# Kernel tuning notes

Hardware: AMD Instinct MI355X
Metric: run time of the kernel (lower is better)

The kernel has to match this reference:

```python
import jax, jax.numpy as jnp
import numpy as np

B, L, D = 4, 2048, 1024


def setup_inputs() -> dict:
    key = jax.random.key(0)
    ks = jax.random.split(key, 7)
    scale = 1.0 / np.sqrt(D)
    x = jax.random.normal(ks[0], (B, L, D), dtype=jnp.float32)
    wq = jax.random.normal(ks[1], (D, D), dtype=jnp.float32) * scale
    wk = jax.random.normal(ks[2], (D, D), dtype=jnp.float32) * scale
    wv = jax.random.normal(ks[3], (D, D), dtype=jnp.float32) * scale
    bq = jnp.zeros((D,), dtype=jnp.float32)
    bk = jnp.zeros((D,), dtype=jnp.float32)
    bv = jnp.zeros((D,), dtype=jnp.float32)
    # causal decoder mask, shape [B, 1, L, L] as produced by nn.make_causal_mask
    causal = jnp.tril(jnp.ones((L, L), dtype=bool))
    mask = jnp.broadcast_to(causal[None, None, :, :], (B, 1, L, L))
    return {"x": x, "mask": mask, "wq": wq, "bq": bq, "wk": wk, "bk": bk, "wv": wv, "bv": bv}


def reference(x, mask, wq, bq, wk, bk, wv, bv):
    # q/k/v projections (Dense with bias)
    q = x @ wq + bq            # [B, L, D]
    k = x @ wk + bk
    v = x @ wv + bv
    depth = q.shape[-1]
    q = q / jnp.sqrt(jnp.asarray(depth, dtype=q.dtype))
    attn = jnp.einsum('bqd,bkd->bqk', q, k)          # [B, L, L]
    attn = jnp.where(jnp.squeeze(mask), attn, -999999)
    attn = jax.nn.softmax(attn, axis=-1)
    out = attn @ v                                    # [B, L, D]
    return out
```

## Files before the change

### kernel.cpp

```cpp
#include <hip/hip_runtime.h>

typedef __bf16 bf16_t;
typedef __attribute__((ext_vector_type(8))) __bf16 bf16x8;
typedef __attribute__((ext_vector_type(4))) __bf16 bf16x4;
typedef __attribute__((ext_vector_type(4))) float f32x4;

#define B_  4
#define L_  2048
#define D_  1024
#define M_  (B_*L_)
#define N3_ (3*D_)

__device__ __forceinline__ void gload_lds16(const void* g, void* l) {
  __builtin_amdgcn_global_load_lds(
      (__attribute__((address_space(1))) void*)(g),
      (__attribute__((address_space(3))) void*)(l), 16, 0, 0);
}

__device__ __forceinline__ void stage_half(const bf16_t* __restrict__ g, int ld, int grow0,
                                           int k0, bf16_t* lds_tile, int h, int tid) {
  const int lane = tid & 63;
  const int csrc = ((lane & 7) ^ (lane >> 3)) << 3;
  const int rsub = tid >> 3;
  bf16_t* l0 = lds_tile + (size_t)(h * 128 + ((tid >> 6) << 3)) * 64;
  const bf16_t* g0 = g + (size_t)(grow0 + h * 128 + rsub) * ld + (k0 + csrc);
  gload_lds16(g0, l0);
  gload_lds16(g0 + (size_t)64 * ld, l0 + 64 * 64);
}

#define KTILE(J, AC, AN1, AN2, BCr, BNx, bC, bN)                                  \
  do {                                                                            \
    const int j_ = (J);                                                           \
    _Pragma("unroll")                                                             \
    for (int mi = 0; mi < 4; ++mi) {                                              \
      aM1_[mi][0] = *(const bf16x8*)(AC + abase + (4 + mi) * 2048 + co0);         \
      aM1_[mi][1] = *(const bf16x8*)(AC + abase + (4 + mi) * 2048 + co1);         \
    }                                                                             \
    if (j_ + 2 < NT) {                                                            \
      stage_half(A, lda, r0, (j_ + 2) * 64, AN2, 0, tid);                         \
      stage_half(A, lda, r0, (j_ + 2) * 64, AN2, 1, tid);                         \
    }                                                                             \
    asm volatile("s_waitcnt lgkmcnt(8)" ::: "memory");                            \
    __builtin_amdgcn_sched_barrier(0);                                            \
    __builtin_amdgcn_s_setprio(1);                                                \
    _Pragma("unroll")                                                             \
    for (int mi = 0; mi < 4; ++mi)                                                \
      _Pragma("unroll")                                                           \
      for (int ni = 0; ni < 2; ++ni) {                                            \
        acc[mi][ni] = __builtin_amdgcn_mfma_f32_16x16x32_bf16(                    \
            bC[ni][0], aM0_[mi][0], acc[mi][ni], 0, 0, 0);                        \
        acc[mi][ni] = __builtin_amdgcn_mfma_f32_16x16x32_bf16(                    \
            bC[ni][1], aM0_[mi][1], acc[mi][ni], 0, 0, 0);                        \
      }                                                                           \
    __builtin_amdgcn_s_setprio(0);                                                \
    if (j_ + 2 < NT) asm volatile("s_waitcnt vmcnt(4)" ::: "memory");             \
    else             asm volatile("s_waitcnt vmcnt(0)" ::: "memory");             \
    asm volatile("s_barrier" ::: "memory");                                       \
    if (j_ + 1 < NT) {                                                            \
      _Pragma("unroll")                                                           \
      for (int mi = 0; mi < 4; ++mi) {                                            \
        aM0_[mi][0] = *(const bf16x8*)(AN1 + abase + mi * 2048 + co0);            \
        aM0_[mi][1] = *(const bf16x8*)(AN1 + abase + mi * 2048 + co1);            \
      }                                                                           \
      _Pragma("unroll")                                                           \
      for (int ni = 0; ni < 2; ++ni) {                                            \
        bN[ni][0] = *(const bf16x8*)(BNx + bbase + ni * 1024 + co0);              \
        bN[ni][1] = *(const bf16x8*)(BNx + bbase + ni * 1024 + co1);              \
      }                                                                           \
      if (j_ + 2 < NT)                                                            \
        stage_half(Bt, ldb, c0, (j_ + 2) * 64, BCr, 0, tid);                      \
      asm volatile("s_waitcnt lgkmcnt(12)" ::: "memory");                         \
    } else {                                                                      \
      asm volatile("s_waitcnt lgkmcnt(0)" ::: "memory");                          \
    }                                                                             \
    __builtin_amdgcn_sched_barrier(0);                                            \
    __builtin_amdgcn_s_setprio(1);                                                \
    _Pragma("unroll")                                                             \
    for (int mi = 0; mi < 4; ++mi)                                                \
      _Pragma("unroll")                                                           \
      for (int ni = 0; ni < 2; ++ni) {                                            \
        acc[4 + mi][ni] = __builtin_amdgcn_mfma_f32_16x16x32_bf16(                \
            bC[ni][0], aM1_[mi][0], acc[4 + mi][ni], 0, 0, 0);                    \
        acc[4 + mi][ni] = __builtin_amdgcn_mfma_f32_16x16x32_bf16(                \
            bC[ni][1], aM1_[mi][1], acc[4 + mi][ni], 0, 0, 0);                    \
      }                                                                           \
    __builtin_amdgcn_s_setprio(0);                                                \
    asm volatile("s_barrier" ::: "memory");                                       \
  } while (0)

template<bool OUT_BF16, bool CAUSAL, bool VARK, bool PROJ, bool PVS>
__global__ __launch_bounds__(512, 2)
void gemm8(const bf16_t* __restrict__ A, int lda, long sA,
           const bf16_t* __restrict__ Bt, int ldb, long sB,
           void* __restrict__ Cv, int ldc, long sC,
           float* __restrict__ part,
           const float* __restrict__ b0, const float* __restrict__ b1,
           const float* __restrict__ b2, int K)
{
  const int gx = gridDim.x;
  const int nwg = gx * gridDim.y;
  const int orig = blockIdx.y * gx + blockIdx.x;
  const int swz = (orig & 7) * (nwg >> 3) + (orig >> 3);
  const int bx = swz % gx, yy = swz / gx;

  int by, j0, NT;
  if (PVS) {
    if (yy < 8) { by = yy; const int NTf = 4 * (by + 1); j0 = 0; NT = (by >= 4) ? (NTf >> 1) : NTf; }
    else        { by = yy - 4; const int NTf = 4 * (by + 1); j0 = NTf >> 1; NT = NTf; }
  } else {
    by = yy; j0 = 0;
    const int kend = VARK ? min(K, by * 256 + 256) : K;
    NT = kend >> 6;
  }
  if (CAUSAL && bx > 2 * by + 1) return;

  const int z = blockIdx.z;
  A  += (size_t)z * sA;
  Bt += (size_t)z * sB;

  const int r0 = by * 256, c0 = bx * 128;

  extern __shared__ __align__(16) bf16_t smem[];
  bf16_t* Ab0 = smem;
  bf16_t* Ab1 = smem + 16384;
  bf16_t* Ab2 = smem + 32768;
  bf16_t* Bb0 = smem + 49152;
  bf16_t* Bb1 = smem + 57344;

  const int tid = threadIdx.x;
  const int wid = tid >> 6, lane = tid & 63;
  const int wm = wid >> 2, wn = wid & 3;
  const int rl = lane & 15, cg = lane >> 4, x0 = lane & 7;
  const int co0 = ((cg ^ x0) << 3);
  const int co1 = (((4 + cg) ^ x0) << 3);
  const int abase = (wm * 16 + rl) * 64;
  const int bbase = (wn * 32 + rl) * 64;

  f32x4 acc[8][2] = {};
  bf16x8 aM0_[4][2], aM1_[4][2];
  bf16x8 bA_[2][2], bB_[2][2];

  stage_half(A,  lda, r0, j0 * 64,       Ab0, 0, tid);
  stage_half(A,  lda, r0, j0 * 64,       Ab0, 1, tid);
  stage_half(Bt, ldb, c0, j0 * 64,       Bb0, 0, tid);
  stage_half(A,  lda, r0, (j0 + 1) * 64, Ab1, 0, tid);
  stage_half(A,  lda, r0, (j0 + 1) * 64, Ab1, 1, tid);
  stage_half(Bt, ldb, c0, (j0 + 1) * 64, Bb1, 0, tid);
  asm volatile("s_waitcnt vmcnt(6)" ::: "memory");
  asm volatile("s_barrier" ::: "memory");
  #pragma unroll
  for (int mi = 0; mi < 4; ++mi) {
    aM0_[mi][0] = *(const bf16x8*)(Ab0 + abase + mi * 2048 + co0);
    aM0_[mi][1] = *(const bf16x8*)(Ab0 + abase + mi * 2048 + co1);
  }
  #pragma unroll
  for (int ni = 0; ni < 2; ++ni) {
    bA_[ni][0] = *(const bf16x8*)(Bb0 + bbase + ni * 1024 + co0);
    bA_[ni][1] = *(const bf16x8*)(Bb0 + bbase + ni * 1024 + co1);
  }

  bf16_t *A0 = Ab0, *A1 = Ab1, *A2 = Ab2;
  for (int j = j0; j < NT; j += 2) {
    KTILE(j,     A0, A1, A2, Bb0, Bb1, bA_, bB_);
    KTILE(j + 1, A1, A2, A0, Bb1, Bb0, bB_, bA_);
    bf16_t* t = A2; A2 = A1; A1 = A0; A0 = t;
  }

  const int ml = lane & 15, ng = cg * 4;
  #pragma unroll
  for (int mi = 0; mi < 8; ++mi) {
    const int r = r0 + mi * 32 + wm * 16 + ml;
    #pragma unroll
    for (int ni = 0; ni < 2; ++ni) {
      const int c = c0 + wn * 32 + ni * 16 + ng;
      f32x4 v = acc[mi][ni];
      if (PROJ) {
        const float* bias = (c < D_) ? b0 : (c < 2 * D_) ? b1 : b2;
        const float4 bb = *(const float4*)(bias + (c & (D_ - 1)));
        const float sc = (c < D_) ? 0.03125f : 1.0f;
        v[0] = (v[0] + bb.x) * sc; v[1] = (v[1] + bb.y) * sc;
        v[2] = (v[2] + bb.z) * sc; v[3] = (v[3] + bb.w) * sc;
      }
      if (PVS) {
        float* dst = (yy < 8)
            ? (float*)Cv + (size_t)z * sC + (size_t)r * ldc + c
            : part + (size_t)z * (1024 * 1024) + (size_t)(r - 1024) * 1024 + c;
        *(f32x4*)dst = v;
      } else if (OUT_BF16) {
        bf16x4 o = {(bf16_t)v[0], (bf16_t)v[1], (bf16_t)v[2], (bf16_t)v[3]};
        *(bf16x4*)((bf16_t*)Cv + (size_t)z * sC + (size_t)r * ldc + c) = o;
      } else {
        *(f32x4*)((float*)Cv + (size_t)z * sC + (size_t)r * ldc + c) = v;
      }
    }
  }
}

__global__ void add_partial(float* __restrict__ out, const float* __restrict__ part) {
  const int i = blockIdx.x * blockDim.x + threadIdx.x;
  const int z = i >> 18;
  const int o = i & 262143;
  float4* dst = (float4*)(out + (size_t)z * L_ * D_ + 1024 * D_) + o;
  const float4 p = ((const float4*)(part + (size_t)z * 1024 * 1024))[o];
  float4 d = *dst;
  d.x += p.x; d.y += p.y; d.z += p.z; d.w += p.w;
  *dst = d;
}

__device__ __forceinline__ float blk_red_max(float v, float* red, int lane, int wid) {
  #pragma unroll
  for (int o = 32; o; o >>= 1) v = fmaxf(v, __shfl_down(v, o));
  __syncthreads();
  if (lane == 0) red[wid] = v;
  __syncthreads();
  return fmaxf(fmaxf(red[0], red[1]), fmaxf(red[2], red[3]));
}
__device__ __forceinline__ float blk_red_sum(float v, float* red, int lane, int wid) {
  #pragma unroll
  for (int o = 32; o; o >>= 1) v += __shfl_down(v, o);
  __syncthreads();
  if (lane == 0) red[wid] = v;
  __syncthreads();
  return red[0] + red[1] + red[2] + red[3];
}

__global__ __launch_bounds__(256)
void softmax_causal(const bf16_t* __restrict__ S, bf16_t* __restrict__ P) {
  const int r = blockIdx.x;
  const int n = r + 1;
  const int kend = min(((n + 255) >> 8) << 8, L_);
  const bf16_t* row = S + (size_t)blockIdx.y * L_ * L_ + (size_t)r * L_;
  bf16_t* prow = P + (size_t)blockIdx.y * L_ * L_ + (size_t)r * L_;
  const int tid = threadIdx.x, lane = tid & 63, wid = tid >> 6;
  const int c0 = tid * 8;
  __shared__ float red[4];

  const bf16x8 v8 = *(const bf16x8*)(row + c0);
  float s[8];
  #pragma unroll
  for (int i = 0; i < 8; ++i)
    s[i] = (c0 + i < n) ? (float)v8[i] : -3.402823466e38f;

  float mx = s[0];
  #pragma unroll
  for (int i = 1; i < 8; ++i) mx = fmaxf(mx, s[i]);
  mx = blk_red_max(mx, red, lane, wid);

  float e[8]; float sum = 0.f;
  #pragma unroll
  for (int i = 0; i < 8; ++i) {
    const float v = (c0 + i < n) ? __expf(s[i] - mx) : 0.f;
    e[i] = v; sum += v;
  }
  sum = blk_red_sum(sum, red, lane, wid);
  const float inv = 1.0f / sum;

  if (c0 < kend) {
    bf16x8 o;
    #pragma unroll
    for (int i = 0; i < 8; ++i) o[i] = (bf16_t)(e[i] * inv);
    *(bf16x8*)(prow + c0) = o;
  }
}

__global__ void cvt_f32_bf16(const float* __restrict__ in, bf16_t* __restrict__ out, int n4) {
  const int stride = gridDim.x * blockDim.x;
  for (int i = blockIdx.x * blockDim.x + threadIdx.x; i < n4; i += stride) {
    const float4 v = ((const float4*)in)[i];
    bf16x4 o = { (bf16_t)v.x, (bf16_t)v.y, (bf16_t)v.z, (bf16_t)v.w };
    ((bf16x4*)out)[i] = o;
  }
}

__global__ void transpose_w3(const float* __restrict__ w0, const float* __restrict__ w1,
                             const float* __restrict__ w2, bf16_t* __restrict__ oT) {
  const float* w = blockIdx.z == 0 ? w0 : (blockIdx.z == 1 ? w1 : w2);
  bf16_t* o = oT + (size_t)blockIdx.z * D_ * D_;
  __shared__ float t[32][33];
  const int tx = threadIdx.x, ty = threadIdx.y;
  const int x  = blockIdx.x * 32 + tx;
  const int y0 = blockIdx.y * 32;
  #pragma unroll
  for (int j = 0; j < 4; ++j)
    t[ty + j * 8][tx] = w[(size_t)(y0 + ty + j * 8) * D_ + x];
  __syncthreads();
  const int x2 = y0 + tx;
  const int y2 = blockIdx.x * 32;
  #pragma unroll
  for (int j = 0; j < 4; ++j)
    o[(size_t)(y2 + ty + j * 8) * D_ + x2] = (bf16_t)t[tx][ty + j * 8];
}

__global__ void transpose_bf16(const bf16_t* __restrict__ in, int ld_in, int coff,
                               bf16_t* __restrict__ out, int R, int C) {
  __shared__ bf16_t t[32][34];
  const int tx = threadIdx.x, ty = threadIdx.y;
  const int x  = blockIdx.x * 32 + tx;
  const int y0 = blockIdx.y * 32;
  #pragma unroll
  for (int j = 0; j < 4; ++j)
    t[ty + j * 8][tx] = in[(size_t)(y0 + ty + j * 8) * ld_in + coff + x];
  __syncthreads();
  const int x2 = y0 + tx;
  const int y2 = blockIdx.x * 32;
  #pragma unroll
  for (int j = 0; j < 4; ++j)
    out[(size_t)(y2 + ty + j * 8) * R + x2] = t[tx][ty + j * 8];
}

extern "C" void kernel_launch(void* const* d_in, const int* in_sizes, int n_in,
                              void* d_out, int out_size, void* d_ws, size_t ws_size,
                              hipStream_t stream) {
  const float* x  = (const float*)d_in[0];
  const float* wq = (const float*)d_in[2];
  const float* bq = (const float*)d_in[3];
  const float* wk = (const float*)d_in[4];
  const float* bk = (const float*)d_in[5];
  const float* wv = (const float*)d_in[6];
  const float* bv = (const float*)d_in[7];
  float* out = (float*)d_out;

  bf16_t* xb   = (bf16_t*)d_ws;
  bf16_t* wT   = xb  + (size_t)M_ * D_;
  bf16_t* qkv  = wT  + (size_t)N3_ * D_;
  bf16_t* vbT  = qkv + (size_t)M_ * N3_;
  bf16_t* Sb   = vbT + (size_t)M_ * D_;
  bf16_t* Pfull = qkv;
  float*  part = (float*)Sb;

  const size_t SMEM = 131072;

  cvt_f32_bf16<<<1024, 256, 0, stream>>>(x, xb, M_ * D_ / 4);
  transpose_w3<<<dim3(32, 32, 3), dim3(32, 8), 0, stream>>>(wq, wk, wv, wT);

  gemm8<true, false, false, true, false><<<dim3(N3_ / 128, M_ / 256), 512, SMEM, stream>>>(
      xb, D_, 0, wT, D_, 0, qkv, N3_, 0, nullptr, bq, bk, bv, D_);

  transpose_bf16<<<dim3(D_ / 32, M_ / 32), dim3(32, 8), 0, stream>>>(qkv, N3_, 2 * D_, vbT, M_, D_);

  gemm8<true, true, false, false, false><<<dim3(L_ / 128, L_ / 256, B_), 512, SMEM, stream>>>(
      qkv, N3_, (long)L_ * N3_, qkv + D_, N3_, (long)L_ * N3_, Sb, L_, (long)L_ * L_,
      nullptr, nullptr, nullptr, nullptr, D_);

  softmax_causal<<<dim3(L_, B_), 256, 0, stream>>>(Sb, Pfull);

  gemm8<false, false, false, false, true><<<dim3(D_ / 128, 12, B_), 512, SMEM, stream>>>(
      Pfull, L_, (long)L_ * L_, vbT, M_, (long)L_, out, D_, (long)L_ * D_,
      part, nullptr, nullptr, nullptr, L_);

  add_partial<<<4096, 256, 0, stream>>>(out, part);
}
```

Baseline: 189.1 us.

## Rebalance causal PV GEMM into equal-work jobs with paired bands and split-K

Replaces the PV GEMM's 12-row grid, where the four largest bands were split in half, with an 8-row job table. Each job does about 16-20 k-tiles of work: short bands are paired with long ones in a single workgroup, and only bands 5-7 are split, with their partial sums written to a scratch buffer. The aim is to even out per-workgroup work, drop the grid from 384 to 256 workgroups, and shrink the partial buffer and the add_partial pass. The cost is that some workgroups run two segments back to back, which adds prologue and epilogue overhead, and the hardcoded table relies on band 5-7 partial writes never overlapping.

Measured after the change: 332.1 us. +75.6%, slower.

```diff
diff --git a/kernel.cpp b/kernel.cpp
--- a/kernel.cpp
+++ b/kernel.cpp
@@ -88,10 +88,10 @@
     asm volatile("s_barrier" ::: "memory");                                       \
   } while (0)
 
-template<bool OUT_BF16, bool CAUSAL, bool VARK, bool PROJ, bool PVS>
+template<bool OUT_BF16, bool CAUSAL, bool VARK, bool PROJ, bool PVJOB>
 __global__ __launch_bounds__(512, 2)
-void gemm8(const bf16_t* __restrict__ A, int lda, long sA,
-           const bf16_t* __restrict__ Bt, int ldb, long sB,
+void gemm8(const bf16_t* __restrict__ A_, int lda, long sA,
+           const bf16_t* __restrict__ Bt_, int ldb, long sB,
            void* __restrict__ Cv, int ldc, long sC,
            float* __restrict__ part,
            const float* __restrict__ b0, const float* __restrict__ b1,
@@ -101,24 +101,34 @@
   const int nwg = gx * gridDim.y;
   const int orig = blockIdx.y * gx + blockIdx.x;
   const int swz = (orig & 7) * (nwg >> 3) + (orig >> 3);
-  const int bx = swz % gx, yy = swz / gx;
-
-  int by, j0, NT;
-  if (PVS) {
-    if (yy < 8) { by = yy; const int NTf = 4 * (by + 1); j0 = 0; NT = (by >= 4) ? (NTf >> 1) : NTf; }
-    else        { by = yy - 4; const int NTf = 4 * (by + 1); j0 = NTf >> 1; NT = NTf; }
+  const int bx = swz % gx, by = swz / gx;
+  if (CAUSAL && bx > 2 * by + 1) return;
+
+  const int z = blockIdx.z;
+  const bf16_t* A  = A_  + (size_t)z * sA;
+  const bf16_t* Bt = Bt_ + (size_t)z * sB;
+
+  const int c0 = bx * 128;
+
+  int nseg = 1, sband0 = by, sj00 = 0, snt0, sband1 = 0, sj01 = 0, snt1 = 0;
+  bool topart = false;
+  if (PVJOB) {
+    switch (by) {
+      case 0:  sband0 = 3; sj00 = 0;  snt0 = 16; break;
+      case 1:  sband0 = 4; sj00 = 0;  snt0 = 20; break;
+      case 2:  nseg = 2; sband0 = 0; sj00 = 0; snt0 = 4;
+               sband1 = 7; sj01 = 0; snt1 = 14; break;
+      case 3:  sband0 = 7; sj00 = 14; snt0 = 32; topart = true; break;
+      case 4:  nseg = 2; sband0 = 1; sj00 = 0; snt0 = 8;
+               sband1 = 6; sj01 = 0; snt1 = 10; break;
+      case 5:  sband0 = 6; sj00 = 10; snt0 = 28; topart = true; break;
+      case 6:  nseg = 2; sband0 = 2; sj00 = 0; snt0 = 12;
+               sband1 = 5; sj01 = 0; snt1 = 6; break;
+      default: sband0 = 5; sj00 = 6;  snt0 = 24; topart = true; break;
+    }
   } else {
-    by = yy; j0 = 0;
-    const int kend = VARK ? min(K, by * 256 + 256) : K;
-    NT = kend >> 6;
+    snt0 = (VARK ? min(K, by * 256 + 256) : K) >> 6;
   }
-  if (CAUSAL && bx > 2 * by + 1) return;
-
-  const int z = blockIdx.z;
-  A  += (size_t)z * sA;
-  Bt += (size_t)z * sB;
-
-  const int r0 = by * 256, c0 = bx * 128;
 
   extern __shared__ __align__(16) bf16_t smem[];
   bf16_t* Ab0 = smem;
@@ -136,72 +146,80 @@
   const int abase = (wm * 16 + rl) * 64;
   const int bbase = (wn * 32 + rl) * 64;
 
-  f32x4 acc[8][2] = {};
-  bf16x8 aM0_[4][2], aM1_[4][2];
-  bf16x8 bA_[2][2], bB_[2][2];
-
-  stage_half(A,  lda, r0, j0 * 64,       Ab0, 0, tid);
-  stage_half(A,  lda, r0, j0 * 64,       Ab0, 1, tid);
-  stage_half(Bt, ldb, c0, j0 * 64,       Bb0, 0, tid);
-  stage_half(A,  lda, r0, (j0 + 1) * 64, Ab1, 0, tid);
-  stage_half(A,  lda, r0, (j0 + 1) * 64, Ab1, 1, tid);
-  stage_half(Bt, ldb, c0, (j0 + 1) * 64, Bb1, 0, tid);
-  asm volatile("s_waitcnt vmcnt(6)" ::: "memory");
-  asm volatile("s_barrier" ::: "memory");
-  #pragma unroll
-  for (int mi = 0; mi < 4; ++mi) {
-    aM0_[mi][0] = *(const bf16x8*)(Ab0 + abase + mi * 2048 + co0);
-    aM0_[mi][1] = *(const bf16x8*)(Ab0 + abase + mi * 2048 + co1);
-  }
-  #pragma unroll
-  for (int ni = 0; ni < 2; ++ni) {
-    bA_[ni][0] = *(const bf16x8*)(Bb0 + bbase + ni * 1024 + co0);
-    bA_[ni][1] = *(const bf16x8*)(Bb0 + bbase + ni * 1024 + co1);
-  }
-
-  bf16_t *A0 = Ab0, *A1 = Ab1, *A2 = Ab2;
-  for (int j = j0; j < NT; j += 2) {
-    KTILE(j,     A0, A1, A2, Bb0, Bb1, bA_, bB_);
-    KTILE(j + 1, A1, A2, A0, Bb1, Bb0, bB_, bA_);
-    bf16_t* t = A2; A2 = A1; A1 = A0; A0 = t;
-  }
-
-  const int ml = lane & 15, ng = cg * 4;
-  #pragma unroll
-  for (int mi = 0; mi < 8; ++mi) {
-    const int r = r0 + mi * 32 + wm * 16 + ml;
+  auto run_seg = [&](int bandv, int j0, int NTv, bool pwrite) {
+    const int r0 = bandv * 256;
+    const int NT = NTv;
+
+    f32x4 acc[8][2] = {};
+    bf16x8 aM0_[4][2], aM1_[4][2];
+    bf16x8 bA_[2][2], bB_[2][2];
+
+    stage_half(A,  lda, r0, j0 * 64,       Ab0, 0, tid);
+    stage_half(A,  lda, r0, j0 * 64,       Ab0, 1, tid);
+    stage_half(Bt, ldb, c0, j0 * 64,       Bb0, 0, tid);
+    stage_half(A,  lda, r0, (j0 + 1) * 64, Ab1, 0, tid);
+    stage_half(A,  lda, r0, (j0 + 1) * 64, Ab1, 1, tid);
+    stage_half(Bt, ldb, c0, (j0 + 1) * 64, Bb1, 0, tid);
+    asm volatile("s_waitcnt vmcnt(6)" ::: "memory");
+    asm volatile("s_barrier" ::: "memory");
+    #pragma unroll
+    for (int mi = 0; mi < 4; ++mi) {
+      aM0_[mi][0] = *(const bf16x8*)(Ab0 + abase + mi * 2048 + co0);
+      aM0_[mi][1] = *(const bf16x8*)(Ab0 + abase + mi * 2048 + co1);
+    }
     #pragma unroll
     for (int ni = 0; ni < 2; ++ni) {
-      const int c = c0 + wn * 32 + ni * 16 + ng;
-      f32x4 v = acc[mi][ni];
-      if (PROJ) {
-        const float* bias = (c < D_) ? b0 : (c < 2 * D_) ? b1 : b2;
-        const float4 bb = *(const float4*)(bias + (c & (D_ - 1)));
-        const float sc = (c < D_) ? 0.03125f : 1.0f;
-        v[0] = (v[0] + bb.x) * sc; v[1] = (v[1] + bb.y) * sc;
-        v[2] = (v[2] + bb.z) * sc; v[3] = (v[3] + bb.w) * sc;
+      bA_[ni][0] = *(const bf16x8*)(Bb0 + bbase + ni * 1024 + co0);
+      bA_[ni][1] = *(const bf16x8*)(Bb0 + bbase + ni * 1024 + co1);
+    }
+
+    bf16_t *A0 = Ab0, *A1 = Ab1, *A2 = Ab2;
+    for (int j = j0; j < NT; j += 2) {
+      KTILE(j,     A0, A1, A2, Bb0, Bb1, bA_, bB_);
+      KTILE(j + 1, A1, A2, A0, Bb1, Bb0, bB_, bA_);
+      bf16_t* t = A2; A2 = A1; A1 = A0; A0 = t;
+    }
+
+    const int ml = lane & 15, ng = cg * 4;
+    #pragma unroll
+    for (int mi = 0; mi < 8; ++mi) {
+      const int r = r0 + mi * 32 + wm * 16 + ml;
+      #pragma unroll
+      for (int ni = 0; ni < 2; ++ni) {
+        const int c = c0 + wn * 32 + ni * 16 + ng;
+        f32x4 v = acc[mi][ni];
+        if (PROJ) {
+          const float* bias = (c < D_) ? b0 : (c < 2 * D_) ? b1 : b2;
+          const float4 bb = *(const float4*)(bias + (c & (D_ - 1)));
+          const float sc = (c < D_) ? 0.03125f : 1.0f;
+          v[0] = (v[0] + bb.x) * sc; v[1] = (v[1] + bb.y) * sc;
+          v[2] = (v[2] + bb.z) * sc; v[3] = (v[3] + bb.w) * sc;
+        }
+        if (PVJOB) {
+          float* dst = pwrite
+              ? part + (size_t)z * (768 * 1024) + (size_t)(r - 1280) * 1024 + c
+              : (float*)Cv + (size_t)z * sC + (size_t)r * ldc + c;
+          *(f32x4*)dst = v;
+        } else if (OUT_BF16) {
+          bf16x4 o = {(bf16_t)v[0], (bf16_t)v[1], (bf16_t)v[2], (bf16_t)v[3]};
+          *(bf16x4*)((bf16_t*)Cv + (size_t)z * sC + (size_t)r * ldc + c) = o;
+        } else {
+          *(f32x4*)((float*)Cv + (size_t)z * sC + (size_t)r * ldc + c) = v;
+        }
       }
-      if (PVS) {
-        float* dst = (yy < 8)
-            ? (float*)Cv + (size_t)z * sC + (size_t)r * ldc + c
-            : part + (size_t)z * (1024 * 1024) + (size_t)(r - 1024) * 1024 + c;
-        *(f32x4*)dst = v;
-      } else if (OUT_BF16) {
-        bf16x4 o = {(bf16_t)v[0], (bf16_t)v[1], (bf16_t)v[2], (bf16_t)v[3]};
-        *(bf16x4*)((bf16_t*)Cv + (size_t)z * sC + (size_t)r * ldc + c) = o;
-      } else {
-        *(f32x4*)((float*)Cv + (size_t)z * sC + (size_t)r * ldc + c) = v;
-      }
-    }
-  }
+    }
+  };
+
+  run_seg(sband0, sj00, snt0, topart);
+  if (PVJOB && nseg == 2) run_seg(sband1, sj01, snt1, false);
 }
 
 __global__ void add_partial(float* __restrict__ out, const float* __restrict__ part) {
   const int i = blockIdx.x * blockDim.x + threadIdx.x;
-  const int z = i >> 18;
-  const int o = i & 262143;
-  float4* dst = (float4*)(out + (size_t)z * L_ * D_ + 1024 * D_) + o;
-  const float4 p = ((const float4*)(part + (size_t)z * 1024 * 1024))[o];
+  const int z = i / 196608;
+  const int o = i - z * 196608;
+  float4* dst = (float4*)(out + (size_t)z * L_ * D_ + 1280 * D_) + o;
+  const float4 p = ((const float4*)(part + (size_t)z * 768 * 1024))[o];
   float4 d = *dst;
   d.x += p.x; d.y += p.y; d.z += p.z; d.w += p.w;
   *dst = d;
@@ -344,9 +362,9 @@
 
   softmax_causal<<<dim3(L_, B_), 256, 0, stream>>>(Sb, Pfull);
 
-  gemm8<false, false, false, false, true><<<dim3(D_ / 128, 12, B_), 512, SMEM, stream>>>(
+  gemm8<false, false, false, false, true><<<dim3(8, 8, B_), 512, SMEM, stream>>>(
       Pfull, L_, (long)L_ * L_, vbT, M_, (long)L_, out, D_, (long)L_ * D_,
       part, nullptr, nullptr, nullptr, L_);
 
-  add_partial<<<4096, 256, 0, stream>>>(out, part);
-}
+  add_partial<<<3072, 256, 0, stream>>>(out, part);
+}
```
